# Kernel tuning notes

Measured on AMD Instinct MI355X. Metric: run time of the kernel, lower is better.

## Reference

```python
import jax, jax.numpy as jnp
import numpy as np

FORGET_BIAS = 1.0  # tf.nn.rnn_cell.LSTMCell default
HIDDEN = 64


def setup_inputs() -> dict:
    key = jax.random.key(0)
    k1, k2 = jax.random.split(key)
    B, T, D = 4096, 9, 512
    x = jax.random.normal(k1, (B, T, D), dtype=jnp.float32)
    # Fused LSTM kernel: [(D + H), 4H], gate order (i, j, f, o) as in TF LSTMCell
    kernel = jax.random.normal(k2, (D + HIDDEN, 4 * HIDDEN), dtype=jnp.float32) * 0.02
    bias = jnp.zeros((4 * HIDDEN,), dtype=jnp.float32)
    return {"x": x, "kernel": kernel, "bias": bias}


def _lstm_scan(x, kernel, bias):
    B, T, D = x.shape
    H = HIDDEN
    # Split kernel into input and recurrent parts for a cleaner scan body.
    Wx = kernel[:D]          # [D, 4H]
    Wh = kernel[D:]          # [H, 4H]
    # Precompute input contributions for all timesteps in one big GEMM.
    xg = jnp.einsum('btd,dg->btg', x, Wx) + bias  # [B, T, 4H]

    def step(carry, xg_t):
        c, h = carry
        gates = xg_t + h @ Wh  # [B, 4H]
        i, j, f, o = jnp.split(gates, 4, axis=-1)  # TF gate order: i, j, f, o
        c_new = jax.nn.sigmoid(f + FORGET_BIAS) * c + jax.nn.sigmoid(i) * jnp.tanh(j)
        h_new = jax.nn.sigmoid(o) * jnp.tanh(c_new)
        return (c_new, h_new), h_new

    c0 = jnp.zeros((B, H), dtype=x.dtype)
    h0 = jnp.zeros((B, H), dtype=x.dtype)
    _, hs = jax.lax.scan(step, (c0, h0), jnp.swapaxes(xg, 0, 1))  # hs: [T, B, H]
    return jnp.transpose(hs, (1, 0, 2))  # [B, T, H]


def reference(x, kernel, bias):
    return _lstm_scan(x, kernel, bias)
```

## Files before the change

### kernel.cpp

```cpp
#include <hip/hip_runtime.h>
#include <math.h>

#define T_STEPS 9
#define D_IN    512
#define HID     64
#define G4      256
#define BPB     8
#define ROWS    72

typedef short  short8 __attribute__((ext_vector_type(8)));
typedef float  f32x4  __attribute__((ext_vector_type(4)));
typedef unsigned int uint;
typedef unsigned short ushort;

__device__ __forceinline__ ushort f2bf(float f) {
    uint u = __float_as_uint(f);
    u = (u + 0x7FFFu + ((u >> 16) & 1u)) >> 16;
    return (ushort)u;
}
__device__ __forceinline__ float fsig(float x) {
    return 1.0f / (1.0f + __expf(-x));
}
__device__ __forceinline__ float ftanh(float x) {
    float t = __expf(-2.0f * fabsf(x));
    float r = (1.0f - t) / (1.0f + t);
    return copysignf(r, x);
}

__global__ __launch_bounds__(256)
void prep_w(const float* __restrict__ kern, ushort* __restrict__ wxT,
            ushort* __restrict__ whT)
{
    int i = blockIdx.x * 256 + threadIdx.x;
    if (i < 131072) {
        int j  = i & 7;
        int n  = (i >> 3) & 255;
        int qk = (i >> 11) & 3;
        int k0 = i >> 13;
        int k  = k0 * 32 + qk * 8 + j;
        wxT[i] = f2bf(kern[(size_t)k * G4 + n]);
    } else {
        int i2 = i - 131072;
        int j  = i2 & 7;
        int n  = (i2 >> 3) & 255;
        int kq = i2 >> 11;
        whT[i2] = f2bf(kern[(size_t)(D_IN + kq * 8 + j) * G4 + n]);
    }
}

__global__ __launch_bounds__(256, 2)
void lstm_fused(const float* __restrict__ x, const ushort* __restrict__ wxT,
                const ushort* __restrict__ whT, const float* __restrict__ bias,
                float* __restrict__ out)
{
    __shared__ ushort sAm[80 * 512];
    ushort* const sH = &sAm[72 * 512];

    const int t = threadIdx.x;
    const int w = t >> 6, l = t & 63;
    const int lane15 = l & 15, quad = l >> 4;
    const int u = w * 16 + lane15;

    {
        uint4 z = {0u, 0u, 0u, 0u};
        ((uint4*)&sAm[72 * 512])[t]       = z;
        ((uint4*)&sAm[72 * 512])[t + 256] = z;
    }

    short8 bFb[2][4];
    {
        const ushort* wxc = wxT + (size_t)(0 * 4 + quad) * 256 * 8;
        #pragma unroll
        for (int g = 0; g < 4; ++g)
            bFb[0][g] = *(const short8*)&wxc[(size_t)(g * 64 + u) * 8];
    }

    const float4* xblk = (const float4*)(x + (size_t)blockIdx.x * (ROWS * D_IN));
    #pragma unroll
    for (int h = 0; h < 2; ++h) {
        float4 v[18];
        #pragma unroll
        for (int q = 0; q < 18; ++q)
            v[q] = xblk[(h * 18 + q) * 256 + t];
        #pragma unroll
        for (int q = 0; q < 18; ++q) {
            int flat = (h * 18 + q) * 256 + t;
            int r    = flat >> 7;
            int colq = flat & 127;
            int b = r / 9, s = r - b * 9;
            int row = s * 8 + b;
            int kq  = colq >> 1;
            int adr = row * 512 + ((kq ^ (row & 7)) << 3) + ((colq & 1) << 2);
            uint2 p;
            p.x = f2bf(v[q].x) | ((uint)f2bf(v[q].y) << 16);
            p.y = f2bf(v[q].z) | ((uint)f2bf(v[q].w) << 16);
            *(uint2*)&sAm[adr] = p;
        }
    }
    __syncthreads();

    f32x4 acc[5][4];
    #pragma unroll
    for (int i = 0; i < 5; ++i)
        #pragma unroll
        for (int g = 0; g < 4; ++g)
            acc[i][g] = (f32x4){0.f, 0.f, 0.f, 0.f};

    #pragma unroll
    for (int k = 0; k < 16; ++k) {
        if (k < 15) {
            const ushort* wxc = wxT + (size_t)((k + 1) * 4 + quad) * 256 * 8;
            #pragma unroll
            for (int g = 0; g < 4; ++g)
                bFb[(k + 1) & 1][g] = *(const short8*)&wxc[(size_t)(g * 64 + u) * 8];
        }
        #pragma unroll
        for (int i = 0; i < 5; ++i) {
            int row = i * 16 + lane15;
            short8 aF = *(const short8*)
                &sAm[row * 512 + (((k * 4 + quad) ^ (row & 7)) << 3)];
            #pragma unroll
            for (int g = 0; g < 4; ++g)
                acc[i][g] = __builtin_amdgcn_mfma_f32_16x16x32_bf16(aF, bFb[k & 1][g], acc[i][g], 0, 0, 0);
        }
    }

    short8 whF[4][2];
    #pragma unroll
    for (int g = 0; g < 4; ++g)
        #pragma unroll
        for (int kh = 0; kh < 2; ++kh)
            whF[g][kh] = *(const short8*)&whT[(size_t)((kh * 4 + quad) * 256 + g * 64 + u) * 8];

    float bia[4];
    bia[0] = bias[u];
    bia[1] = bias[64 + u];
    bia[2] = bias[128 + u] + 1.0f;
    bia[3] = bias[192 + u];

    float cst[4] = {0.f, 0.f, 0.f, 0.f};
    const int b0 = blockIdx.x * BPB;

    #pragma unroll
    for (int s = 0; s < T_STEPS; ++s) {
        const int  i = s >> 1;
        const int  p = s & 1;
        const bool active = ((quad >> 1) == p);
        const int  bofs = (quad & 1) * 4;

        f32x4 g4[4];
        #pragma unroll
        for (int g = 0; g < 4; ++g)
            #pragma unroll
            for (int r = 0; r < 4; ++r)
                g4[g][r] = acc[i][g][r] + bia[g];

        short8 aF[2];
        #pragma unroll
        for (int kh = 0; kh < 2; ++kh)
            aF[kh] = *(const short8*)&sH[((kh * 4 + quad) * 16 + lane15) * 8];

        #pragma unroll
        for (int g = 0; g < 4; ++g)
            #pragma unroll
            for (int kh = 0; kh < 2; ++kh)
                g4[g] = __builtin_amdgcn_mfma_f32_16x16x32_bf16(aF[kh], whF[g][kh], g4[g], 0, 0, 0);

        __syncthreads();

        const int wrow = 8 * ((s + 1) & 1);
        #pragma unroll
        for (int r = 0; r < 4; ++r) {
            float cp = __shfl_xor(cst[r], 32);
            if (active) {
                float ii = fsig(g4[0][r]);
                float jj = ftanh(g4[1][r]);
                float ff = fsig(g4[2][r]);
                float oo = fsig(g4[3][r]);
                float c  = ff * cp + ii * jj;
                cst[r] = c;
                float h = oo * ftanh(c);
                int bb = bofs + r;
                out[((size_t)(b0 + bb) * T_STEPS + s) * HID + u] = h;
                sH[((u >> 3) * 16 + wrow + bb) * 8 + (u & 7)] = f2bf(h);
            }
        }
        __syncthreads();
    }
}

extern "C" void kernel_launch(void* const* d_in, const int* in_sizes, int n_in,
                              void* d_out, int out_size, void* d_ws, size_t ws_size,
                              hipStream_t stream)
{
    const float* x    = (const float*)d_in[0];
    const float* kern = (const float*)d_in[1];
    const float* bias = (const float*)d_in[2];
    float* out = (float*)d_out;

    const int B = in_sizes[0] / (T_STEPS * D_IN);

    ushort* wxT = (ushort*)d_ws;
    ushort* whT = (ushort*)((char*)d_ws + 262144);

    prep_w<<<576, 256, 0, stream>>>(kern, wxT, whT);
    lstm_fused<<<B / BPB, 256, 0, stream>>>(x, wxT, whT, bias, out);
}
```

Baseline: 127.9 us.

## Stream x directly into MFMA registers and halve batch rows per block

Drops the large LDS staging buffer for x: each lane now loads its fp32 x fragments straight from global memory, converts them to bf16 in registers and feeds the MFMAs, with a software-prefetched next k-slice. The batch per block falls from 8 to 4, so the row tiles drop from 5 to 3, the recurrent phase rotates through four quads per tile, and occupancy hint rises to 4 blocks/CU. This targets the LDS staging/sync cost and LDS-limited occupancy, at the price of uncoalesced strided global loads, redundant wx loads across twice as many blocks, and a padded third tile that wastes MFMA work.

Measured after the change: 177.1 us. 1.38x slower.

```diff
diff --git a/kernel.cpp b/kernel.cpp
--- a/kernel.cpp
+++ b/kernel.cpp
@@ -5,8 +5,8 @@
 #define D_IN    512
 #define HID     64
 #define G4      256
-#define BPB     8
-#define ROWS    72
+#define BPB     4
+#define ROWS    36
 
 typedef short  short8 __attribute__((ext_vector_type(8)));
 typedef float  f32x4  __attribute__((ext_vector_type(4)));
@@ -25,6 +25,14 @@
     float t = __expf(-2.0f * fabsf(x));
     float r = (1.0f - t) / (1.0f + t);
     return copysignf(r, x);
+}
+__device__ __forceinline__ short8 cvt8(float4 a, float4 b) {
+    union { uint4 u; short8 s; } r;
+    r.u.x = f2bf(a.x) | ((uint)f2bf(a.y) << 16);
+    r.u.y = f2bf(a.z) | ((uint)f2bf(a.w) << 16);
+    r.u.z = f2bf(b.x) | ((uint)f2bf(b.y) << 16);
+    r.u.w = f2bf(b.z) | ((uint)f2bf(b.w) << 16);
+    return r.s;
 }
 
 __global__ __launch_bounds__(256)
@@ -48,80 +56,66 @@
     }
 }
 
-__global__ __launch_bounds__(256, 2)
+__global__ __launch_bounds__(256, 4)
 void lstm_fused(const float* __restrict__ x, const ushort* __restrict__ wxT,
                 const ushort* __restrict__ whT, const float* __restrict__ bias,
                 float* __restrict__ out)
 {
-    __shared__ ushort sAm[80 * 512];
-    ushort* const sH = &sAm[72 * 512];
+    __shared__ ushort sH[8 * 16 * 8];
 
     const int t = threadIdx.x;
     const int w = t >> 6, l = t & 63;
     const int lane15 = l & 15, quad = l >> 4;
     const int u = w * 16 + lane15;
 
-    {
-        uint4 z = {0u, 0u, 0u, 0u};
-        ((uint4*)&sAm[72 * 512])[t]       = z;
-        ((uint4*)&sAm[72 * 512])[t + 256] = z;
-    }
-
-    short8 bFb[2][4];
-    {
-        const ushort* wxc = wxT + (size_t)(0 * 4 + quad) * 256 * 8;
-        #pragma unroll
-        for (int g = 0; g < 4; ++g)
-            bFb[0][g] = *(const short8*)&wxc[(size_t)(g * 64 + u) * 8];
-    }
-
-    const float4* xblk = (const float4*)(x + (size_t)blockIdx.x * (ROWS * D_IN));
-    #pragma unroll
-    for (int h = 0; h < 2; ++h) {
-        float4 v[18];
-        #pragma unroll
-        for (int q = 0; q < 18; ++q)
-            v[q] = xblk[(h * 18 + q) * 256 + t];
-        #pragma unroll
-        for (int q = 0; q < 18; ++q) {
-            int flat = (h * 18 + q) * 256 + t;
-            int r    = flat >> 7;
-            int colq = flat & 127;
-            int b = r / 9, s = r - b * 9;
-            int row = s * 8 + b;
-            int kq  = colq >> 1;
-            int adr = row * 512 + ((kq ^ (row & 7)) << 3) + ((colq & 1) << 2);
-            uint2 p;
-            p.x = f2bf(v[q].x) | ((uint)f2bf(v[q].y) << 16);
-            p.y = f2bf(v[q].z) | ((uint)f2bf(v[q].w) << 16);
-            *(uint2*)&sAm[adr] = p;
-        }
-    }
-    __syncthreads();
-
-    f32x4 acc[5][4];
-    #pragma unroll
-    for (int i = 0; i < 5; ++i)
+    ((uint2*)sH)[t] = (uint2){0u, 0u};
+
+    const char* xb = (const char*)(x + (size_t)blockIdx.x * (BPB * T_STEPS * D_IN));
+    const int sq = lane15 >> 2, bq = lane15 & 3;
+    int vo[3];
+    vo[0] = (bq * 9 + sq) * 2048 + quad * 32;
+    vo[1] = (bq * 9 + 4 + sq) * 2048 + quad * 32;
+    vo[2] = ((lane15 < 4) ? (lane15 * 9 + 8) : 35) * 2048 + quad * 32;
+
+    f32x4 acc[3][4];
+    #pragma unroll
+    for (int i = 0; i < 3; ++i)
         #pragma unroll
         for (int g = 0; g < 4; ++g)
             acc[i][g] = (f32x4){0.f, 0.f, 0.f, 0.f};
 
+    float4 rx[3][2];
+    #pragma unroll
+    for (int i = 0; i < 3; ++i) {
+        rx[i][0] = *(const float4*)(xb + vo[i]);
+        rx[i][1] = *(const float4*)(xb + vo[i] + 16);
+    }
+    short8 bF[4];
+    #pragma unroll
+    for (int g = 0; g < 4; ++g)
+        bF[g] = *(const short8*)&wxT[(size_t)(quad * 256 + g * 64 + u) * 8];
+
     #pragma unroll
     for (int k = 0; k < 16; ++k) {
+        short8 aF[3];
+        #pragma unroll
+        for (int i = 0; i < 3; ++i) aF[i] = cvt8(rx[i][0], rx[i][1]);
         if (k < 15) {
-            const ushort* wxc = wxT + (size_t)((k + 1) * 4 + quad) * 256 * 8;
+            #pragma unroll
+            for (int i = 0; i < 3; ++i) {
+                rx[i][0] = *(const float4*)(xb + vo[i] + (k + 1) * 128);
+                rx[i][1] = *(const float4*)(xb + vo[i] + (k + 1) * 128 + 16);
+            }
+        }
+        #pragma unroll
+        for (int i = 0; i < 3; ++i)
             #pragma unroll
             for (int g = 0; g < 4; ++g)
-                bFb[(k + 1) & 1][g] = *(const short8*)&wxc[(size_t)(g * 64 + u) * 8];
-        }
-        #pragma unroll
-        for (int i = 0; i < 5; ++i) {
-            int row = i * 16 + lane15;
-            short8 aF = *(const short8*)
-                &sAm[row * 512 + (((k * 4 + quad) ^ (row & 7)) << 3)];
+                acc[i][g] = __builtin_amdgcn_mfma_f32_16x16x32_bf16(aF[i], bF[g], acc[i][g], 0, 0, 0);
+        if (k < 15) {
             #pragma unroll
             for (int g = 0; g < 4; ++g)
-                acc[i][g] = __builtin_amdgcn_mfma_f32_16x16x32_bf16(aF, bFb[k & 1][g], acc[i][g], 0, 0, 0);
+                bF[g] = *(const short8*)&wxT[(size_t)(((k + 1) * 4 + quad) * 256 + g * 64 + u) * 8];
         }
     }
 
@@ -140,38 +134,40 @@
 
     float cst[4] = {0.f, 0.f, 0.f, 0.f};
     const int b0 = blockIdx.x * BPB;
+    const int srcl = (((quad + 3) & 3) << 4) + lane15;
+
+    __syncthreads();
 
     #pragma unroll
     for (int s = 0; s < T_STEPS; ++s) {
-        const int  i = s >> 1;
-        const int  p = s & 1;
-        const bool active = ((quad >> 1) == p);
-        const int  bofs = (quad & 1) * 4;
+        const int  itile = s >> 2;
+        const int  phase = s & 3;
+        const bool active = (quad == phase);
 
         f32x4 g4[4];
         #pragma unroll
         for (int g = 0; g < 4; ++g)
             #pragma unroll
             for (int r = 0; r < 4; ++r)
-                g4[g][r] = acc[i][g][r] + bia[g];
-
-        short8 aF[2];
+                g4[g][r] = acc[itile][g][r] + bia[g];
+
+        short8 aFh[2];
         #pragma unroll
         for (int kh = 0; kh < 2; ++kh)
-            aF[kh] = *(const short8*)&sH[((kh * 4 + quad) * 16 + lane15) * 8];
+            aFh[kh] = *(const short8*)&sH[((kh * 4 + quad) * 16 + lane15) * 8];
 
         #pragma unroll
         for (int g = 0; g < 4; ++g)
             #pragma unroll
             for (int kh = 0; kh < 2; ++kh)
-                g4[g] = __builtin_amdgcn_mfma_f32_16x16x32_bf16(aF[kh], whF[g][kh], g4[g], 0, 0, 0);
+                g4[g] = __builtin_amdgcn_mfma_f32_16x16x32_bf16(aFh[kh], whF[g][kh], g4[g], 0, 0, 0);
 
         __syncthreads();
 
-        const int wrow = 8 * ((s + 1) & 1);
+        const int wrow = ((s + 1) & 3) * 4;
         #pragma unroll
         for (int r = 0; r < 4; ++r) {
-            float cp = __shfl_xor(cst[r], 32);
+            float cp = __shfl(cst[r], srcl);
             if (active) {
                 float ii = fsig(g4[0][r]);
                 float jj = ftanh(g4[1][r]);
@@ -180,9 +176,8 @@
                 float c  = ff * cp + ii * jj;
                 cst[r] = c;
                 float h = oo * ftanh(c);
-                int bb = bofs + r;
-                out[((size_t)(b0 + bb) * T_STEPS + s) * HID + u] = h;
-                sH[((u >> 3) * 16 + wrow + bb) * 8 + (u & 7)] = f2bf(h);
+                out[((size_t)(b0 + r) * T_STEPS + s) * HID + u] = h;
+                sH[((u >> 3) * 16 + wrow + r) * 8 + (u & 7)] = f2bf(h);
             }
         }
         __syncthreads();
```
